# Performance work log

Measured on AMD Instinct MI355X. Metric: run time of the kernel, lower is better.

The kernel has to match this reference:

```python
import jax, jax.numpy as jnp
import numpy as np

N = 8192
E = 262144


def gcn_layer(x, w, row, col, edge_weight, n_nodes):
    # support = x @ W ; out = A_sparse @ support (COO spmm via segment_sum)
    support = x @ w                              # [N, d_out]
    msg = support[col] * edge_weight[:, None]    # gather + scale, [E, d_out]
    return jax.ops.segment_sum(msg, row, num_segments=n_nodes)  # [N, d_out]


def setup_inputs() -> dict:
    key = jax.random.key(0)
    k1, k2, k3, k4, k5, k6 = jax.random.split(key, 6)
    x = jax.random.normal(k1, (N, 512), dtype=jnp.float32)
    w1 = jax.random.normal(k2, (512, 256), dtype=jnp.float32) * 0.05
    w2 = jax.random.normal(k3, (256, 16), dtype=jnp.float32) * 0.05
    edge_weight = jax.random.uniform(k4, (E,), dtype=jnp.float32)
    row = jax.random.randint(k5, (E,), 0, N, dtype=jnp.int32)
    col = jax.random.randint(k6, (E,), 0, N, dtype=jnp.int32)
    return {"x": x, "w1": w1, "w2": w2, "edge_weight": edge_weight,
            "row": row, "col": col}


def reference(x, w1, w2, edge_weight, row, col):
    # gc1: dropout(identity at eval) -> linear -> spmm -> relu
    h1 = jax.nn.relu(gcn_layer(x, w1, row, col, edge_weight, N))
    # gc2: identity activation
    z = gcn_layer(h1, w2, row, col, edge_weight, N)          # [N, 16]
    # InnerProductDecoder with act = identity (dropout off at eval)
    adj = z @ z.T                                            # [N, N]
    return adj
```

## Files before the change

### kernel.cpp

```cpp
#include <hip/hip_runtime.h>
#include <hip/hip_bf16.h>

#define NN 8192
#define NE 262144
#define DIN 512
#define DH 256
#define DZ 16
#define CAP 96

typedef __attribute__((ext_vector_type(8))) short bf16x8;
typedef __attribute__((ext_vector_type(4))) float f32x4;

__device__ __forceinline__ ushort f2bf(float f) {
    __hip_bfloat16 h = __float2bfloat16(f);
    return *(ushort*)&h;
}
__device__ __forceinline__ float bf2f(ushort h) {
    return __uint_as_float((uint)h << 16);
}

__global__ void k_prep_zero(const float* __restrict__ W, ushort* __restrict__ WBf,
                            int* __restrict__ count) {
    int b = blockIdx.x;
    int t = threadIdx.x;
    if (b < 512) {
        int o = b * 256 + t;
        int n = o >> 9, k = o & 511;
        WBf[o] = f2bf(W[(size_t)k * DH + n]);
    } else {
        count[(b - 512) * 256 + t] = 0;
    }
}

__global__ __launch_bounds__(256) void k_gemm1_scatter(
    const float* __restrict__ X, const ushort* __restrict__ W1T,
    ushort* __restrict__ O,
    const int* __restrict__ ROW, const int* __restrict__ COL,
    const float* __restrict__ EW, int* __restrict__ count,
    int* __restrict__ col_s, float* __restrict__ w_s) {
    int t = threadIdx.x;
    {
        int gid0 = blockIdx.x * 256 + t;
#pragma unroll
        for (int it = 0; it < 2; ++it) {
            int e = gid0 + it * 131072;
            int r = ROW[e];
            int slot = atomicAdd(&count[r], 1);
            if (slot < CAP) {
                col_s[r * CAP + slot] = COL[e];
                w_s[r * CAP + slot]   = EW[e];
            }
        }
    }
    int wave = t >> 6, lane = t & 63;
    int m0 = blockIdx.x * 16;
    int fr = lane & 15, fg = lane >> 4;
    f32x4 acc[4] = {};
    const float* xrow = &X[(size_t)(m0 + fr) * DIN];
    for (int k0 = 0; k0 < DIN; k0 += 64) {
#pragma unroll
        for (int kk = 0; kk < 2; ++kk) {
            const float* xp = &xrow[k0 + kk * 32 + fg * 8];
            float4 f0 = *(const float4*)&xp[0];
            float4 f1 = *(const float4*)&xp[4];
            ushort ua[8] = {f2bf(f0.x), f2bf(f0.y), f2bf(f0.z), f2bf(f0.w),
                            f2bf(f1.x), f2bf(f1.y), f2bf(f1.z), f2bf(f1.w)};
            bf16x8 af = *(const bf16x8*)&ua[0];
#pragma unroll
            for (int j = 0; j < 4; ++j) {
                bf16x8 bb = *(const bf16x8*)&W1T[(size_t)(wave * 64 + j * 16 + fr) * DIN +
                                                 k0 + kk * 32 + fg * 8];
                acc[j] = __builtin_amdgcn_mfma_f32_16x16x32_bf16(af, bb, acc[j], 0, 0, 0);
            }
        }
    }
#pragma unroll
    for (int j = 0; j < 4; ++j)
#pragma unroll
        for (int r = 0; r < 4; ++r)
            O[(size_t)(m0 + fg * 4 + r) * DH + wave * 64 + j * 16 + fr] = f2bf(acc[j][r]);
}

__global__ __launch_bounds__(256) void k_spmm1_gemm2(const ushort* __restrict__ Sbf,
                                                     const int* __restrict__ count,
                                                     const int* __restrict__ cs,
                                                     const float* __restrict__ wsrt,
                                                     const float* __restrict__ W2,
                                                     float* __restrict__ S2) {
    __shared__ float w2s[DH * DZ];
    __shared__ float hs[4][DH];
    __shared__ int   ecs[4][CAP];
    __shared__ float ews[4][CAP];
    int t = threadIdx.x;
#pragma unroll
    for (int i = t; i < DH * DZ / 4; i += 256)
        ((float4*)w2s)[i] = ((const float4*)W2)[i];
    int wave = t >> 6, lane = t & 63;
    int r = blockIdx.x * 4 + wave;
    int nv = min(count[r], CAP);
    int e0 = r * CAP;
    if (lane < nv) { ecs[wave][lane] = cs[e0 + lane]; ews[wave][lane] = wsrt[e0 + lane]; }
    int l2i = lane + 64;
    if (l2i < nv) { ecs[wave][l2i] = cs[e0 + l2i]; ews[wave][l2i] = wsrt[e0 + l2i]; }
    float ax[4] = {}, ay[4] = {};
    int e = 0;
    for (; e + 15 < nv; e += 16) {
        uint2 p[16];
        float w[16];
#pragma unroll
        for (int q = 0; q < 16; ++q) {
            int kq = ecs[wave][e + q];
            w[q] = ews[wave][e + q];
            p[q] = *(const uint2*)&Sbf[(size_t)kq * DH + lane * 4];
        }
#pragma unroll
        for (int q = 0; q < 16; q += 2) {
            ax[0] += w[q] * bf2f((ushort)p[q].x);
            ax[1] += w[q] * bf2f((ushort)(p[q].x >> 16));
            ax[2] += w[q] * bf2f((ushort)p[q].y);
            ax[3] += w[q] * bf2f((ushort)(p[q].y >> 16));
            ay[0] += w[q + 1] * bf2f((ushort)p[q + 1].x);
            ay[1] += w[q + 1] * bf2f((ushort)(p[q + 1].x >> 16));
            ay[2] += w[q + 1] * bf2f((ushort)p[q + 1].y);
            ay[3] += w[q + 1] * bf2f((ushort)(p[q + 1].y >> 16));
        }
    }
    for (; e + 3 < nv; e += 4) {
        uint2 p[4];
        float w[4];
#pragma unroll
        for (int q = 0; q < 4; ++q) {
            int kq = ecs[wave][e + q];
            w[q] = ews[wave][e + q];
            p[q] = *(const uint2*)&Sbf[(size_t)kq * DH + lane * 4];
        }
#pragma unroll
        for (int q = 0; q < 4; q += 2) {
            ax[0] += w[q] * bf2f((ushort)p[q].x);
            ax[1] += w[q] * bf2f((ushort)(p[q].x >> 16));
            ax[2] += w[q] * bf2f((ushort)p[q].y);
            ax[3] += w[q] * bf2f((ushort)(p[q].y >> 16));
            ay[0] += w[q + 1] * bf2f((ushort)p[q + 1].x);
            ay[1] += w[q + 1] * bf2f((ushort)(p[q + 1].x >> 16));
            ay[2] += w[q + 1] * bf2f((ushort)p[q + 1].y);
            ay[3] += w[q + 1] * bf2f((ushort)(p[q + 1].y >> 16));
        }
    }
    for (; e < nv; ++e) {
        float w0 = ews[wave][e];
        uint2 p0 = *(const uint2*)&Sbf[(size_t)ecs[wave][e] * DH + lane * 4];
        ax[0] += w0 * bf2f((ushort)p0.x); ax[1] += w0 * bf2f((ushort)(p0.x >> 16));
        ax[2] += w0 * bf2f((ushort)p0.y); ax[3] += w0 * bf2f((ushort)(p0.y >> 16));
    }
    float4 h;
    h.x = fmaxf(ax[0] + ay[0], 0.f);
    h.y = fmaxf(ax[1] + ay[1], 0.f);
    h.z = fmaxf(ax[2] + ay[2], 0.f);
    h.w = fmaxf(ax[3] + ay[3], 0.f);
    *(float4*)&hs[wave][lane * 4] = h;
    __syncthreads();
    int jj = lane >> 2, g = lane & 3;
    float acc = 0.f;
    int kb = g * 64;
#pragma unroll 8
    for (int k = kb; k < kb + 64; ++k) acc += hs[wave][k] * w2s[k * DZ + jj];
    acc += __shfl_xor(acc, 1);
    acc += __shfl_xor(acc, 2);
    if (g == 0) S2[(size_t)r * DZ + jj] = acc;
}

__global__ __launch_bounds__(256) void k_spmm2(const float* __restrict__ S2,
                                               const int* __restrict__ count,
                                               const int* __restrict__ cs,
                                               const float* __restrict__ wsrt,
                                               ushort* __restrict__ ZHi,
                                               ushort* __restrict__ ZLo) {
    int t = threadIdx.x;
    int rl = t >> 4, c = t & 15;
    int r = blockIdx.x * 16 + rl;
    int nv = min(count[r], CAP);
    int e0 = r * CAP;
    float a0 = 0.f, a1 = 0.f, a2 = 0.f, a3 = 0.f;
    int e = 0;
    for (; e + 7 < nv; e += 8) {
        float v[8], w[8];
#pragma unroll
        for (int q = 0; q < 8; ++q) {
            int kq = cs[e0 + e + q];
            w[q] = wsrt[e0 + e + q];
            v[q] = S2[(size_t)kq * DZ + c];
        }
        a0 += w[0] * v[0] + w[4] * v[4];
        a1 += w[1] * v[1] + w[5] * v[5];
        a2 += w[2] * v[2] + w[6] * v[6];
        a3 += w[3] * v[3] + w[7] * v[7];
    }
    for (; e < nv; ++e) a0 += wsrt[e0 + e] * S2[(size_t)cs[e0 + e] * DZ + c];
    float acc = (a0 + a1) + (a2 + a3);
    ushort h = f2bf(acc);
    ZHi[(size_t)r * DZ + c] = h;
    ZLo[(size_t)r * DZ + c] = f2bf(acc - bf2f(h));
}

__global__ __launch_bounds__(256) void k_gemm3_mfma(const ushort* __restrict__ ZHi,
                                                    const ushort* __restrict__ ZLo,
                                                    float* __restrict__ O) {
    int t = threadIdx.x;
    int wave = t >> 6, lane = t & 63;
    int rb = blockIdx.y * 128 + (wave >> 1) * 64;
    int cb = blockIdx.x * 128 + (wave & 1) * 64;
    int fr = lane & 15, fg = lane >> 4;
    int ko = (fg & 1) * 8;
    const ushort* asel = (fg < 2) ? ZHi : ZLo;

    bf16x8 cpack[4], rhi[4], rlo[4];
    bf16x8 zero8 = {};
#pragma unroll
    for (int j = 0; j < 4; ++j)
        cpack[j] = *(const bf16x8*)&asel[(size_t)(cb + j * 16 + fr) * DZ + ko];
#pragma unroll
    for (int i = 0; i < 4; ++i) {
        rhi[i] = *(const bf16x8*)&ZHi[(size_t)(rb + i * 16 + fr) * DZ + ko];
        rlo[i] = (fg < 2) ? *(const bf16x8*)&ZLo[(size_t)(rb + i * 16 + fr) * DZ + ko]
                          : zero8;
    }
    f32x4 acc[4][4] = {};
#pragma unroll
    for (int i = 0; i < 4; ++i)
#pragma unroll
        for (int j = 0; j < 4; ++j) {
            acc[i][j] = __builtin_amdgcn_mfma_f32_16x16x32_bf16(cpack[j], rhi[i],
                                                                acc[i][j], 0, 0, 0);
            acc[i][j] = __builtin_amdgcn_mfma_f32_16x16x32_bf16(cpack[j], rlo[i],
                                                                acc[i][j], 0, 0, 0);
        }
#pragma unroll
    for (int i = 0; i < 4; ++i)
#pragma unroll
        for (int j = 0; j < 4; ++j)
            *(f32x4*)&O[(size_t)(rb + i * 16 + fr) * NN + cb + j * 16 + fg * 4] = acc[i][j];
}

extern "C" void kernel_launch(void* const* d_in, const int* in_sizes, int n_in,
                              void* d_out, int out_size, void* d_ws, size_t ws_size,
                              hipStream_t stream) {
    const float* x  = (const float*)d_in[0];
    const float* w1 = (const float*)d_in[1];
    const float* w2 = (const float*)d_in[2];
    const float* ew = (const float*)d_in[3];
    const int*  row = (const int*)d_in[4];
    const int*  col = (const int*)d_in[5];
    float* out = (float*)d_out;

    char* ws = (char*)d_ws;
    int*    count = (int*)ws;
    ushort* zhi   = (ushort*)(ws + 73728);
    ushort* zlo   = (ushort*)(ws + 73728 + 262144);

    char* ob = (char*)d_out;
    ushort* support1 = (ushort*)ob;
    float*  s2       = (float*)(ob + 16u * 1024 * 1024);
    int*    col_s    = (int*)(ob + 24u * 1024 * 1024);
    float*  w_s      = (float*)(ob + 28u * 1024 * 1024);
    ushort* w1tbf    = (ushort*)(ob + 36u * 1024 * 1024);

    k_prep_zero<<<544, 256, 0, stream>>>(w1, w1tbf, count);
    k_gemm1_scatter<<<NN / 16, 256, 0, stream>>>(x, w1tbf, support1,
                                                 row, col, ew, count, col_s, w_s);
    k_spmm1_gemm2<<<NN / 4, 256, 0, stream>>>(support1, count, col_s, w_s, w2, s2);
    k_spmm2<<<NN / 16, 256, 0, stream>>>(s2, count, col_s, w_s, zhi, zlo);
    k_gemm3_mfma<<<dim3(NN / 128, NN / 128), 256, 0, stream>>>(zhi, zlo, out);
}
```

Measured before the change: 120.0 us.

## Split GEMM1 over N halves with LDS-staged A tile; nontemporal output stores

The first GEMM+scatter kernel now launches 1024 blocks instead of 512. Each block covers 16 rows and half of the 256 output columns. The X tile is converted to bf16 once into shared memory rather than reloaded by every wave, and each block scatters one edge per thread. The goal is more parallelism and less redundant global X traffic, at the cost of reading X twice across the column halves. The final 8192x8192 output is also written with nontemporal stores to avoid cache pollution.

```diff
diff --git a/kernel.cpp b/kernel.cpp
--- a/kernel.cpp
+++ b/kernel.cpp
@@ -38,47 +38,54 @@
     const int* __restrict__ ROW, const int* __restrict__ COL,
     const float* __restrict__ EW, int* __restrict__ count,
     int* __restrict__ col_s, float* __restrict__ w_s) {
-    int t = threadIdx.x;
+    __shared__ ushort As[16][520];
+    int t = threadIdx.x;
+    int b = blockIdx.x;
     {
-        int gid0 = blockIdx.x * 256 + t;
-#pragma unroll
-        for (int it = 0; it < 2; ++it) {
-            int e = gid0 + it * 131072;
-            int r = ROW[e];
-            int slot = atomicAdd(&count[r], 1);
-            if (slot < CAP) {
-                col_s[r * CAP + slot] = COL[e];
-                w_s[r * CAP + slot]   = EW[e];
-            }
-        }
-    }
+        int e = b * 256 + t;
+        int r = ROW[e];
+        int slot = atomicAdd(&count[r], 1);
+        if (slot < CAP) {
+            col_s[r * CAP + slot] = COL[e];
+            w_s[r * CAP + slot]   = EW[e];
+        }
+    }
+    int mb = b >> 1, nb = b & 1;
+    int m0 = mb * 16;
+#pragma unroll
+    for (int uix = 0; uix < 4; ++uix) {
+        int u = uix * 256 + t;
+        int urow = u >> 6;
+        int ucol = (u & 63) * 8;
+        const float* xp = &X[(size_t)(m0 + urow) * DIN + ucol];
+        float4 f0 = *(const float4*)&xp[0];
+        float4 f1 = *(const float4*)&xp[4];
+        ushort ua[8] = {f2bf(f0.x), f2bf(f0.y), f2bf(f0.z), f2bf(f0.w),
+                        f2bf(f1.x), f2bf(f1.y), f2bf(f1.z), f2bf(f1.w)};
+        *(bf16x8*)&As[urow][ucol] = *(const bf16x8*)&ua[0];
+    }
+    __syncthreads();
     int wave = t >> 6, lane = t & 63;
-    int m0 = blockIdx.x * 16;
     int fr = lane & 15, fg = lane >> 4;
-    f32x4 acc[4] = {};
-    const float* xrow = &X[(size_t)(m0 + fr) * DIN];
+    int n0 = nb * 128 + wave * 32;
+    f32x4 acc[2] = {};
     for (int k0 = 0; k0 < DIN; k0 += 64) {
 #pragma unroll
         for (int kk = 0; kk < 2; ++kk) {
-            const float* xp = &xrow[k0 + kk * 32 + fg * 8];
-            float4 f0 = *(const float4*)&xp[0];
-            float4 f1 = *(const float4*)&xp[4];
-            ushort ua[8] = {f2bf(f0.x), f2bf(f0.y), f2bf(f0.z), f2bf(f0.w),
-                            f2bf(f1.x), f2bf(f1.y), f2bf(f1.z), f2bf(f1.w)};
-            bf16x8 af = *(const bf16x8*)&ua[0];
-#pragma unroll
-            for (int j = 0; j < 4; ++j) {
-                bf16x8 bb = *(const bf16x8*)&W1T[(size_t)(wave * 64 + j * 16 + fr) * DIN +
+            bf16x8 af = *(const bf16x8*)&As[fr][k0 + kk * 32 + fg * 8];
+#pragma unroll
+            for (int j = 0; j < 2; ++j) {
+                bf16x8 bb = *(const bf16x8*)&W1T[(size_t)(n0 + j * 16 + fr) * DIN +
                                                  k0 + kk * 32 + fg * 8];
                 acc[j] = __builtin_amdgcn_mfma_f32_16x16x32_bf16(af, bb, acc[j], 0, 0, 0);
             }
         }
     }
 #pragma unroll
-    for (int j = 0; j < 4; ++j)
+    for (int j = 0; j < 2; ++j)
 #pragma unroll
         for (int r = 0; r < 4; ++r)
-            O[(size_t)(m0 + fg * 4 + r) * DH + wave * 64 + j * 16 + fr] = f2bf(acc[j][r]);
+            O[(size_t)(m0 + fg * 4 + r) * DH + n0 + j * 16 + fr] = f2bf(acc[j][r]);
 }
 
 __global__ __launch_bounds__(256) void k_spmm1_gemm2(const ushort* __restrict__ Sbf,
@@ -238,7 +245,8 @@
     for (int i = 0; i < 4; ++i)
 #pragma unroll
         for (int j = 0; j < 4; ++j)
-            *(f32x4*)&O[(size_t)(rb + i * 16 + fr) * NN + cb + j * 16 + fg * 4] = acc[i][j];
+            __builtin_nontemporal_store(
+                acc[i][j], (f32x4*)&O[(size_t)(rb + i * 16 + fr) * NN + cb + j * 16 + fg * 4]);
 }
 
 extern "C" void kernel_launch(void* const* d_in, const int* in_sizes, int n_in,
@@ -265,8 +273,8 @@
     ushort* w1tbf    = (ushort*)(ob + 36u * 1024 * 1024);
 
     k_prep_zero<<<544, 256, 0, stream>>>(w1, w1tbf, count);
-    k_gemm1_scatter<<<NN / 16, 256, 0, stream>>>(x, w1tbf, support1,
-                                                 row, col, ew, count, col_s, w_s);
+    k_gemm1_scatter<<<1024, 256, 0, stream>>>(x, w1tbf, support1,
+                                              row, col, ew, count, col_s, w_s);
     k_spmm1_gemm2<<<NN / 4, 256, 0, stream>>>(support1, count, col_s, w_s, w2, s2);
     k_spmm2<<<NN / 16, 256, 0, stream>>>(s2, count, col_s, w_s, zhi, zlo);
     k_gemm3_mfma<<<dim3(NN / 128, NN / 128), 256, 0, stream>>>(zhi, zlo, out);
```

Result: slower. 149.3 us (+24.4%).
